# Kernel optimization log

Hardware: AMD Instinct MI355X
Metric: run time of the kernel (lower is better)

The kernel has to match this reference:

```python
import jax, jax.numpy as jnp
import numpy as np

B, S, H = 2, 2048, 1024
G, HEADS = 4, 16
HPG = HEADS // G          # heads per group = 4
HD = H // HEADS           # head_dim = 64
DG = H // G               # per-group proj dim = 256
SCALE = 1.0 / np.sqrt(HD)


def setup_inputs() -> dict:
    key = jax.random.key(0)
    ks = jax.random.split(key, 6)
    w = 0.02
    return {
        "hidden_states": jax.random.normal(ks[0], (B, S, H), dtype=jnp.float32),
        "Wq": jax.random.normal(ks[1], (G, DG, H), dtype=jnp.float32) * w,
        "bq": jnp.zeros((G, DG), dtype=jnp.float32),
        "Wk": jax.random.normal(ks[2], (G, DG, H), dtype=jnp.float32) * w,
        "bk": jnp.zeros((G, DG), dtype=jnp.float32),
        "Wv": jax.random.normal(ks[3], (G, DG, H), dtype=jnp.float32) * w,
        "bv": jnp.zeros((G, DG), dtype=jnp.float32),
        "Wo": jax.random.normal(ks[4], (H, H), dtype=jnp.float32) * w,
        "bo": jnp.zeros((H,), dtype=jnp.float32),
    }


def _proj_split(x, W, b):
    # x: [B,S,H], W: [G,DG,H], b: [G,DG] -> [B,G,HPG,S,HD]
    y = jnp.einsum("bsh,gdh->bgsd", x, W) + b[None, :, None, :]
    y = y.reshape(x.shape[0], G, x.shape[1], HPG, HD)
    return jnp.transpose(y, (0, 1, 3, 2, 4))


def reference(hidden_states, Wq, bq, Wk, bk, Wv, bv, Wo, bo):
    q = _proj_split(hidden_states, Wq, bq)  # [B,G,HPG,S,HD]
    k = _proj_split(hidden_states, Wk, bk)
    v = _proj_split(hidden_states, Wv, bv)
    scores = jnp.einsum("bghqd,bghkd->bghqk", q, k) * SCALE
    attn = jax.nn.softmax(scores.astype(jnp.float32), axis=-1).astype(v.dtype)
    ctx = jnp.einsum("bghqk,bghkd->bghqd", attn, v)  # [B,G,HPG,S,HD]
    # merge: heads ordered group-major, matching torch cat over group dim
    ctx = jnp.transpose(ctx, (0, 3, 1, 2, 4)).reshape(hidden_states.shape[0], hidden_states.shape[1], H)
    return jnp.einsum("bsh,oh->bso", ctx, Wo) + bo
```

## Files before the change

### kernel.cpp

```cpp
#include <hip/hip_runtime.h>

typedef __bf16 bf16x8 __attribute__((ext_vector_type(8)));
typedef __bf16 bf16x4 __attribute__((ext_vector_type(4)));
typedef short short4v __attribute__((ext_vector_type(4)));
typedef float f32x4 __attribute__((ext_vector_type(4)));

#define LOG2E 1.4426950408889634f

static __device__ __forceinline__ unsigned short f2bf(float f) {
  union { float f; unsigned int u; } c; c.f = f;
  return (unsigned short)((c.u + 0x7fffu + ((c.u >> 16) & 1u)) >> 16);
}

static __device__ __forceinline__ void gload16(const void* g, void* l) {
  __builtin_amdgcn_global_load_lds(
      (const __attribute__((address_space(1))) void*)g,
      (__attribute__((address_space(3))) void*)l, 16, 0, 0);
}

static __device__ __forceinline__ float exp2fast(float x) {
#if __has_builtin(__builtin_amdgcn_exp2f)
  return __builtin_amdgcn_exp2f(x);
#else
  return exp2f(x);
#endif
}

#if __has_builtin(__builtin_amdgcn_mfma_f32_16x16x16bf16_1k)
#define MFMA16_FALLBACK 0
static __device__ __forceinline__ f32x4 mfma16(bf16x4 a, bf16x4 b, f32x4 c) {
  return __builtin_amdgcn_mfma_f32_16x16x16bf16_1k(
      __builtin_bit_cast(short4v, a), __builtin_bit_cast(short4v, b), c, 0, 0, 0);
}
#else
#define MFMA16_FALLBACK 1
static __device__ __forceinline__ f32x4 mfma16(bf16x4 a, bf16x4 b, f32x4 c) {
  f32x4 d;
  asm("s_nop 1\n\tv_mfma_f32_16x16x16_bf16 %0, %1, %2, %3"
      : "=v"(d) : "v"(a), "v"(b), "v"(c));
  return d;
}
#endif

__global__ void cvt_all(const float* __restrict__ x,
                        const float* __restrict__ Wq,
                        const float* __restrict__ Wk,
                        const float* __restrict__ Wv,
                        const float* __restrict__ Wo,
                        ushort4* __restrict__ dst) {
  int i = blockIdx.x * 256 + threadIdx.x;
  const float* src;
  int off;
  if (i < 1048576) {
    src = x; off = i;
  } else {
    int t = (i - 1048576) >> 18;
    off = (i - 1048576) & 262143;
    src = (t == 0) ? Wq : (t == 1) ? Wk : (t == 2) ? Wv : Wo;
  }
  float4 f = ((const float4*)src)[off];
  ushort4 o;
  o.x = f2bf(f.x); o.y = f2bf(f.y); o.z = f2bf(f.z); o.w = f2bf(f.w);
  dst[i] = o;
}

__launch_bounds__(256, 2)
__global__ void qkv_gemm(const unsigned short* __restrict__ xb,
                         const unsigned short* __restrict__ wq,
                         const unsigned short* __restrict__ wk,
                         const unsigned short* __restrict__ wv,
                         const float* __restrict__ bq,
                         const float* __restrict__ bk,
                         const float* __restrict__ bv,
                         unsigned short* __restrict__ Qo,
                         unsigned short* __restrict__ Ko,
                         unsigned short* __restrict__ VTo) {
  __shared__ unsigned short As[128 * 64];
  __shared__ unsigned short Bs[128 * 64];
  const int s0 = blockIdx.x * 128;
  const int n0g = blockIdx.y * 128;
  const int qkv = n0g >> 10;
  const int d0 = n0g & 1023;
  const unsigned short* W = (qkv == 0) ? wq : ((qkv == 1) ? wk : wv);
  const float* bias = (qkv == 0) ? bq : ((qkv == 1) ? bk : bv);

  const unsigned short* Aptr; const unsigned short* Bptr;
  int Aoff, Boff;
  if (qkv < 2) { Aptr = W;  Aoff = d0; Bptr = xb; Boff = s0; }
  else         { Aptr = xb; Aoff = s0; Bptr = W;  Boff = d0; }

  const int tid = threadIdx.x;
  const int lane = tid & 63;
  const int wid = tid >> 6;
  const int wm = (wid >> 1) * 64;
  const int wn = (wid & 1) * 64;
  const int lm = lane & 15;
  const int quad = lane >> 4;

  f32x4 acc[4][4] = {};

  for (int kk = 0; kk < 1024; kk += 64) {
#pragma unroll
    for (int t = 0; t < 4; ++t) {
      int i = t * 256 + tid;
      int row = i >> 3, tp = i & 7;
      int seg = tp ^ (row & 7);
      gload16(Aptr + (size_t)(Aoff + row) * 1024 + kk + seg * 8,
              As + (size_t)i * 8);
      gload16(Bptr + (size_t)(Boff + row) * 1024 + kk + seg * 8,
              Bs + (size_t)i * 8);
    }
    __syncthreads();
#pragma unroll
    for (int h = 0; h < 2; ++h) {
      bf16x8 af[4], bff[4];
#pragma unroll
      for (int mt = 0; mt < 4; ++mt) {
        int r = wm + mt * 16 + lm;
        af[mt] = *(const bf16x8*)(As + r * 64 + (((h * 4 + quad) ^ (r & 7)) * 8));
      }
#pragma unroll
      for (int nt = 0; nt < 4; ++nt) {
        int r = wn + nt * 16 + lm;
        bff[nt] = *(const bf16x8*)(Bs + r * 64 + (((h * 4 + quad) ^ (r & 7)) * 8));
      }
#pragma unroll
      for (int mt = 0; mt < 4; ++mt)
#pragma unroll
        for (int nt = 0; nt < 4; ++nt)
          acc[mt][nt] = __builtin_amdgcn_mfma_f32_16x16x32_bf16(
              af[mt], bff[nt], acc[mt][nt], 0, 0, 0);
    }
    __syncthreads();
  }

  if (qkv < 2) {
    unsigned short* OUT = (qkv == 0) ? Qo : Ko;
    const float scale = (qkv == 0) ? (0.125f * LOG2E) : 1.0f;
#pragma unroll
    for (int mt = 0; mt < 4; ++mt) {
      const int d = d0 + wm + mt * 16 + quad * 4;
      const int g = d >> 8, hpg = (d >> 6) & 3, hd = d & 63;
      const float4 bb = *(const float4*)(bias + d);
#pragma unroll
      for (int nt = 0; nt < 4; ++nt) {
        const int srow = s0 + wn + nt * 16 + lm;
        const int bidx = srow >> 11, s = srow & 2047;
        const int head = (bidx * 4 + g) * 4 + hpg;
        ushort4 o;
        o.x = f2bf((acc[mt][nt][0] + bb.x) * scale);
        o.y = f2bf((acc[mt][nt][1] + bb.y) * scale);
        o.z = f2bf((acc[mt][nt][2] + bb.z) * scale);
        o.w = f2bf((acc[mt][nt][3] + bb.w) * scale);
        *(ushort4*)(OUT + (size_t)head * 131072 + (size_t)s * 64 + hd) = o;
      }
    }
  } else {
#pragma unroll
    for (int nt = 0; nt < 4; ++nt) {
      const int d = d0 + wn + nt * 16 + lm;
      const int g = d >> 8, hpg = (d >> 6) & 3, hd = d & 63;
      const float bb = bias[d];
#pragma unroll
      for (int mt = 0; mt < 4; ++mt) {
        const int sbase = s0 + wm + mt * 16 + quad * 4;
        const int bidx = sbase >> 11, s = sbase & 2047;
        const int head = (bidx * 4 + g) * 4 + hpg;
        ushort4 o;
        o.x = f2bf(acc[mt][nt][0] + bb);
        o.y = f2bf(acc[mt][nt][1] + bb);
        o.z = f2bf(acc[mt][nt][2] + bb);
        o.w = f2bf(acc[mt][nt][3] + bb);
        *(ushort4*)(VTo + (size_t)head * 131072 + (size_t)hd * 2048 + s) = o;
      }
    }
  }
}

static __device__ __forceinline__ void stage_kv(
    const unsigned short* Kh, const unsigned short* Vh, int kv0,
    unsigned short* ksl, unsigned short* vsl, int tid) {
#pragma unroll
  for (int t = 0; t < 4; ++t) {
    int i = t * 256 + tid;
    int slab = i >> 9, kv = (i >> 2) & 127, tp = i & 3;
    int tc = tp ^ ((kv >> 1) & 3);
    gload16(Kh + (size_t)(kv0 + kv) * 64 + slab * 32 + tc * 8, ksl + (size_t)i * 8);
  }
#pragma unroll
  for (int t = 0; t < 4; ++t) {
    int i = t * 256 + tid;
    int hd = i >> 4, tp = i & 15;
    int tc = tp ^ ((hd >> 1) & 7);
    gload16(Vh + (size_t)hd * 2048 + kv0 + tc * 8, vsl + (size_t)i * 8);
  }
}

__launch_bounds__(256, 2)
__global__ void attn_kernel(const unsigned short* __restrict__ Q,
                            const unsigned short* __restrict__ K,
                            const unsigned short* __restrict__ VT,
                            unsigned short* __restrict__ ctx) {
  __shared__ __align__(16) unsigned char smem[65536];

  const int head = blockIdx.y;
  const int q0 = blockIdx.x * 128;
  const int b = head >> 4;
  const int colbase = (head & 15) * 64;

  const unsigned short* Kh = K + (size_t)head * 131072;
  const unsigned short* Vh = VT + (size_t)head * 131072;

  const int tid = threadIdx.x;
  const int lane = tid & 63;
  const int w = tid >> 6;
  const int wq = w & 1;
  const int wkv = w >> 1;
  const int lm = lane & 15;
  const int quad = lane >> 4;

  bf16x8 qf[2][4];
#pragma unroll
  for (int nt = 0; nt < 4; ++nt) {
    const size_t qrow = (size_t)(q0 + wq * 64 + nt * 16 + lm);
#pragma unroll
    for (int c = 0; c < 2; ++c)
      qf[c][nt] = *(const bf16x8*)(Q + (size_t)head * 131072 + qrow * 64 +
                                   c * 32 + quad * 8);
  }

  stage_kv(Kh, Vh, 0, (unsigned short*)smem,
           (unsigned short*)(smem + 32768), tid);
  __syncthreads();

  float psum[4] = {0.f, 0.f, 0.f, 0.f};
  f32x4 oacc[4][4] = {};
  const int kchunk = (quad ^ ((lm >> 1) & 3)) * 8;

  for (int it = 0; it < 16; ++it) {
    const int buf = it & 1;
    const unsigned short* kb = (const unsigned short*)(smem + buf * 16384);
    const unsigned short* vb = (const unsigned short*)(smem + 32768 + buf * 16384);
    if (it < 15)
      stage_kv(Kh, Vh, (it + 1) * 128,
               (unsigned short*)(smem + (buf ^ 1) * 16384),
               (unsigned short*)(smem + 32768 + (buf ^ 1) * 16384), tid);

#pragma unroll
    for (int mt = 0; mt < 4; ++mt) {
      const int kvrow = wkv * 64 + mt * 16 + lm;
      f32x4 s[4] = {};
#pragma unroll
      for (int c = 0; c < 2; ++c) {
        bf16x8 kf = *(const bf16x8*)(kb + c * 4096 + kvrow * 32 + kchunk);
#pragma unroll
        for (int nt = 0; nt < 4; ++nt)
          s[nt] = __builtin_amdgcn_mfma_f32_16x16x32_bf16(kf, qf[c][nt], s[nt],
                                                          0, 0, 0);
      }
      bf16x4 pf[4];
#pragma unroll
      for (int nt = 0; nt < 4; ++nt) {
        float e0 = exp2fast(s[nt][0]), e1 = exp2fast(s[nt][1]);
        float e2 = exp2fast(s[nt][2]), e3 = exp2fast(s[nt][3]);
        psum[nt] += (e0 + e1) + (e2 + e3);
        bf16x4 t;
        t[0] = (__bf16)e0; t[1] = (__bf16)e1; t[2] = (__bf16)e2; t[3] = (__bf16)e3;
        pf[nt] = t;
      }
      const int vgran = ((wkv * 16 + mt * 4 + quad) ^ (lm & 14)) * 4;
#pragma unroll
      for (int hm = 0; hm < 4; ++hm) {
        bf16x4 vf = *(const bf16x4*)(vb + (hm * 16 + lm) * 128 + vgran);
#pragma unroll
        for (int nt = 0; nt < 4; ++nt)
          oacc[hm][nt] = mfma16(vf, pf[nt], oacc[hm][nt]);
      }
    }
    __syncthreads();
  }

#if MFMA16_FALLBACK
  asm volatile("s_nop 7\n\ts_nop 7");
#endif
#pragma unroll
  for (int nt = 0; nt < 4; ++nt) {
    psum[nt] += __shfl_xor(psum[nt], 16, 64);
    psum[nt] += __shfl_xor(psum[nt], 32, 64);
  }

  float* red = (float*)smem;
  float* psred = (float*)(smem + 34816);
  if (wkv == 1) {
#pragma unroll
    for (int nt = 0; nt < 4; ++nt) {
      const int qi = wq * 64 + nt * 16 + lm;
      if (quad == 0) psred[qi] = psum[nt];
#pragma unroll
      for (int hm = 0; hm < 4; ++hm)
        *(f32x4*)(red + qi * 68 + hm * 16 + quad * 4) = oacc[hm][nt];
    }
  }
  __syncthreads();
  if (wkv == 0) {
#pragma unroll
    for (int nt = 0; nt < 4; ++nt) {
      const int qi = wq * 64 + nt * 16 + lm;
      const float inv = 1.0f / (psum[nt] + psred[qi]);
      const size_t row = (size_t)(b * 2048 + q0 + qi);
#pragma unroll
      for (int hm = 0; hm < 4; ++hm) {
        f32x4 o = *(const f32x4*)(red + qi * 68 + hm * 16 + quad * 4);
        o += oacc[hm][nt];
        ushort4 st;
        st.x = f2bf(o[0] * inv);
        st.y = f2bf(o[1] * inv);
        st.z = f2bf(o[2] * inv);
        st.w = f2bf(o[3] * inv);
        *(ushort4*)(ctx + row * 1024 + colbase + hm * 16 + quad * 4) = st;
      }
    }
  }
}

__launch_bounds__(256, 4)
__global__ void out_gemm(const unsigned short* __restrict__ A,
                         const unsigned short* __restrict__ Wb,
                         const float* __restrict__ bo,
                         float* __restrict__ out) {
  __shared__ unsigned short As[128 * 64];
  __shared__ unsigned short Bs[64 * 64];
  const int s0 = blockIdx.x * 64;
  const int o0 = blockIdx.y * 128;

  const int tid = threadIdx.x;
  const int lane = tid & 63;
  const int wid = tid >> 6;
  const int wm = (wid >> 1) * 64;
  const int wn = (wid & 1) * 32;
  const int lm = lane & 15;
  const int quad = lane >> 4;

  f32x4 acc[4][2] = {};

  for (int kk = 0; kk < 1024; kk += 64) {
#pragma unroll
    for (int t = 0; t < 4; ++t) {
      int i = t * 256 + tid;
      int row = i >> 3, tp = i & 7;
      int seg = tp ^ (row & 7);
      gload16(Wb + (size_t)(o0 + row) * 1024 + kk + seg * 8, As + (size_t)i * 8);
    }
#pragma unroll
    for (int t = 0; t < 2; ++t) {
      int i = t * 256 + tid;
      int row = i >> 3, tp = i & 7;
      int seg = tp ^ (row & 7);
      gload16(A + (size_t)(s0 + row) * 1024 + kk + seg * 8, Bs + (size_t)i * 8);
    }
    __syncthreads();
#pragma unroll
    for (int h = 0; h < 2; ++h) {
      bf16x8 af[4], bff[2];
#pragma unroll
      for (int mt = 0; mt < 4; ++mt) {
        int r = wm + mt * 16 + lm;
        af[mt] = *(const bf16x8*)(As + r * 64 + (((h * 4 + quad) ^ (r & 7)) * 8));
      }
#pragma unroll
      for (int nt = 0; nt < 2; ++nt) {
        int r = wn + nt * 16 + lm;
        bff[nt] = *(const bf16x8*)(Bs + r * 64 + (((h * 4 + quad) ^ (r & 7)) * 8));
      }
#pragma unroll
      for (int mt = 0; mt < 4; ++mt)
#pragma unroll
        for (int nt = 0; nt < 2; ++nt)
          acc[mt][nt] = __builtin_amdgcn_mfma_f32_16x16x32_bf16(
              af[mt], bff[nt], acc[mt][nt], 0, 0, 0);
    }
    __syncthreads();
  }

#pragma unroll
  for (int mt = 0; mt < 4; ++mt) {
    const int o = o0 + wm + mt * 16 + quad * 4;
    const float4 bb = *(const float4*)(bo + o);
#pragma unroll
    for (int nt = 0; nt < 2; ++nt) {
      const int s = s0 + wn + nt * 16 + lm;
      float4 v;
      v.x = acc[mt][nt][0] + bb.x;
      v.y = acc[mt][nt][1] + bb.y;
      v.z = acc[mt][nt][2] + bb.z;
      v.w = acc[mt][nt][3] + bb.w;
      *(float4*)(out + (size_t)s * 1024 + o) = v;
    }
  }
}

extern "C" void kernel_launch(void* const* d_in, const int* in_sizes, int n_in,
                              void* d_out, int out_size, void* d_ws, size_t ws_size,
                              hipStream_t stream) {
  const float* x  = (const float*)d_in[0];
  const float* Wq = (const float*)d_in[1];
  const float* bq = (const float*)d_in[2];
  const float* Wk = (const float*)d_in[3];
  const float* bk = (const float*)d_in[4];
  const float* Wv = (const float*)d_in[5];
  const float* bv = (const float*)d_in[6];
  const float* Wo = (const float*)d_in[7];
  const float* bo = (const float*)d_in[8];
  float* out = (float*)d_out;

  char* ws = (char*)d_ws;
  unsigned short* xb  = (unsigned short*)(ws + 0);
  unsigned short* wqb = (unsigned short*)(ws + 8388608);
  unsigned short* wkb = (unsigned short*)(ws + 10485760);
  unsigned short* wvb = (unsigned short*)(ws + 12582912);
  unsigned short* wob = (unsigned short*)(ws + 14680064);
  unsigned short* Qb  = (unsigned short*)(ws + 16777216);
  unsigned short* Kb  = (unsigned short*)(ws + 25165824);
  unsigned short* VTb = (unsigned short*)(ws + 33554432);
  unsigned short* ctxb= (unsigned short*)(ws + 41943040);
  if (ws_size < 50331648) return;

  cvt_all<<<8192, 256, 0, stream>>>(x, Wq, Wk, Wv, Wo, (ushort4*)ws);
  qkv_gemm<<<dim3(32, 24), 256, 0, stream>>>(xb, wqb, wkb, wvb, bq, bk, bv,
                                             Qb, Kb, VTb);
  attn_kernel<<<dim3(16, 32), 256, 0, stream>>>(Qb, Kb, VTb, ctxb);
  out_gemm<<<dim3(64, 8), 256, 0, stream>>>(ctxb, wob, bo, out);
}
```

Measured before the change: 182.4 us.

## Fuse QKV, attention and output GEMM into one persistent kernel with grid barriers

The three compute kernels become device functions called from one persistent kernel of 512 blocks. A software grid barrier built on atomics separates the QKV projection, attention and output projection phases, with the barrier reset inside the conversion kernel. The goal is to remove launch gaps and inter-kernel drains. In exchange, the output GEMM now runs at 2 blocks per CU instead of 4, QKV tiles are imbalanced (768 tiles over 512 blocks), and the barrier relies on all 512 blocks being co-resident, or it deadlocks.

```diff
diff --git a/kernel.cpp b/kernel.cpp
--- a/kernel.cpp
+++ b/kernel.cpp
@@ -42,12 +42,36 @@
 }
 #endif
 
+static __device__ __forceinline__ void grid_barrier(unsigned* bar, unsigned nblk) {
+  __syncthreads();
+  __threadfence();
+  if (threadIdx.x == 0) {
+    unsigned gen = __hip_atomic_load(bar + 1, __ATOMIC_ACQUIRE,
+                                     __HIP_MEMORY_SCOPE_AGENT);
+    unsigned a = __hip_atomic_fetch_add(bar, 1u, __ATOMIC_ACQ_REL,
+                                        __HIP_MEMORY_SCOPE_AGENT);
+    if (a == nblk - 1u) {
+      __hip_atomic_store(bar, 0u, __ATOMIC_RELAXED, __HIP_MEMORY_SCOPE_AGENT);
+      __hip_atomic_store(bar + 1, gen + 1u, __ATOMIC_RELEASE,
+                         __HIP_MEMORY_SCOPE_AGENT);
+    } else {
+      while (__hip_atomic_load(bar + 1, __ATOMIC_ACQUIRE,
+                               __HIP_MEMORY_SCOPE_AGENT) == gen)
+        __builtin_amdgcn_s_sleep(8);
+    }
+  }
+  __threadfence();
+  __syncthreads();
+}
+
 __global__ void cvt_all(const float* __restrict__ x,
                         const float* __restrict__ Wq,
                         const float* __restrict__ Wk,
                         const float* __restrict__ Wv,
                         const float* __restrict__ Wo,
-                        ushort4* __restrict__ dst) {
+                        ushort4* __restrict__ dst,
+                        unsigned* __restrict__ bar) {
+  if (blockIdx.x == 0 && threadIdx.x < 8) bar[threadIdx.x] = 0u;
   int i = blockIdx.x * 256 + threadIdx.x;
   const float* src;
   int off;
@@ -64,21 +88,22 @@
   dst[i] = o;
 }
 
-__launch_bounds__(256, 2)
-__global__ void qkv_gemm(const unsigned short* __restrict__ xb,
-                         const unsigned short* __restrict__ wq,
-                         const unsigned short* __restrict__ wk,
-                         const unsigned short* __restrict__ wv,
-                         const float* __restrict__ bq,
-                         const float* __restrict__ bk,
-                         const float* __restrict__ bv,
-                         unsigned short* __restrict__ Qo,
-                         unsigned short* __restrict__ Ko,
-                         unsigned short* __restrict__ VTo) {
-  __shared__ unsigned short As[128 * 64];
-  __shared__ unsigned short Bs[128 * 64];
-  const int s0 = blockIdx.x * 128;
-  const int n0g = blockIdx.y * 128;
+
+static __device__ void qkv_tile(int tile, unsigned char* smem,
+                                const unsigned short* __restrict__ xb,
+                                const unsigned short* __restrict__ wq,
+                                const unsigned short* __restrict__ wk,
+                                const unsigned short* __restrict__ wv,
+                                const float* __restrict__ bq,
+                                const float* __restrict__ bk,
+                                const float* __restrict__ bv,
+                                unsigned short* __restrict__ Qo,
+                                unsigned short* __restrict__ Ko,
+                                unsigned short* __restrict__ VTo) {
+  unsigned short* As = (unsigned short*)smem;
+  unsigned short* Bs = (unsigned short*)(smem + 16384);
+  const int s0 = (tile & 31) * 128;
+  const int n0g = (tile >> 5) * 128;
   const int qkv = n0g >> 10;
   const int d0 = n0g & 1023;
   const unsigned short* W = (qkv == 0) ? wq : ((qkv == 1) ? wk : wv);
@@ -196,15 +221,13 @@
   }
 }
 
-__launch_bounds__(256, 2)
-__global__ void attn_kernel(const unsigned short* __restrict__ Q,
-                            const unsigned short* __restrict__ K,
-                            const unsigned short* __restrict__ VT,
-                            unsigned short* __restrict__ ctx) {
-  __shared__ __align__(16) unsigned char smem[65536];
-
-  const int head = blockIdx.y;
-  const int q0 = blockIdx.x * 128;
+static __device__ void attn_tile(int tile, unsigned char* smem,
+                                 const unsigned short* __restrict__ Q,
+                                 const unsigned short* __restrict__ K,
+                                 const unsigned short* __restrict__ VT,
+                                 unsigned short* __restrict__ ctx) {
+  const int head = tile >> 4;
+  const int q0 = (tile & 15) * 128;
   const int b = head >> 4;
   const int colbase = (head & 15) * 64;
 
@@ -323,15 +346,15 @@
   }
 }
 
-__launch_bounds__(256, 4)
-__global__ void out_gemm(const unsigned short* __restrict__ A,
-                         const unsigned short* __restrict__ Wb,
-                         const float* __restrict__ bo,
-                         float* __restrict__ out) {
-  __shared__ unsigned short As[128 * 64];
-  __shared__ unsigned short Bs[64 * 64];
-  const int s0 = blockIdx.x * 64;
-  const int o0 = blockIdx.y * 128;
+static __device__ void out_tile(int tile, unsigned char* smem,
+                                const unsigned short* __restrict__ A,
+                                const unsigned short* __restrict__ Wb,
+                                const float* __restrict__ bo,
+                                float* __restrict__ out) {
+  unsigned short* As = (unsigned short*)smem;
+  unsigned short* Bs = (unsigned short*)(smem + 16384);
+  const int s0 = (tile & 63) * 64;
+  const int o0 = (tile >> 6) * 128;
 
   const int tid = threadIdx.x;
   const int lane = tid & 63;
@@ -397,6 +420,36 @@
       *(float4*)(out + (size_t)s * 1024 + o) = v;
     }
   }
+}
+
+__launch_bounds__(256, 2)
+__global__ void fused_kernel(const unsigned short* __restrict__ xb,
+                             const unsigned short* __restrict__ wqb,
+                             const unsigned short* __restrict__ wkb,
+                             const unsigned short* __restrict__ wvb,
+                             const unsigned short* __restrict__ wob,
+                             const float* __restrict__ bq,
+                             const float* __restrict__ bk,
+                             const float* __restrict__ bv,
+                             const float* __restrict__ bo,
+                             unsigned short* __restrict__ Qb,
+                             unsigned short* __restrict__ Kb,
+                             unsigned short* __restrict__ VTb,
+                             unsigned short* __restrict__ ctxb,
+                             float* __restrict__ out,
+                             unsigned* __restrict__ bar) {
+  __shared__ __align__(16) unsigned char smem[65536];
+
+  for (int tile = blockIdx.x; tile < 768; tile += 512)
+    qkv_tile(tile, smem, xb, wqb, wkb, wvb, bq, bk, bv, Qb, Kb, VTb);
+
+  grid_barrier(bar, 512);
+
+  attn_tile(blockIdx.x, smem, Qb, Kb, VTb, ctxb);
+
+  grid_barrier(bar, 512);
+
+  out_tile(blockIdx.x, smem, ctxb, wob, bo, out);
 }
 
 extern "C" void kernel_launch(void* const* d_in, const int* in_sizes, int n_in,
@@ -423,11 +476,11 @@
   unsigned short* Kb  = (unsigned short*)(ws + 25165824);
   unsigned short* VTb = (unsigned short*)(ws + 33554432);
   unsigned short* ctxb= (unsigned short*)(ws + 41943040);
-  if (ws_size < 50331648) return;
-
-  cvt_all<<<8192, 256, 0, stream>>>(x, Wq, Wk, Wv, Wo, (ushort4*)ws);
-  qkv_gemm<<<dim3(32, 24), 256, 0, stream>>>(xb, wqb, wkb, wvb, bq, bk, bv,
-                                             Qb, Kb, VTb);
-  attn_kernel<<<dim3(16, 32), 256, 0, stream>>>(Qb, Kb, VTb, ctxb);
-  out_gemm<<<dim3(64, 8), 256, 0, stream>>>(ctxb, wob, bo, out);
-}
+  unsigned* bar       = (unsigned*)(ws + 50331648);
+  if (ws_size < 50331680) return;
+
+  cvt_all<<<8192, 256, 0, stream>>>(x, Wq, Wk, Wv, Wo, (ushort4*)ws, bar);
+  fused_kernel<<<512, 256, 0, stream>>>(xb, wqb, wkb, wvb, wob,
+                                        bq, bk, bv, bo,
+                                        Qb, Kb, VTb, ctxb, out, bar);
+}
```

Result: slower. 541.4 us (+196.7%).

## Double-buffer LDS tiles in QKV and output GEMMs to overlap loads

Applied to the files above, without the earlier changes.

Both GEMM kernels now keep two LDS buffers per operand. The next k-slice is issued via global_load_lds into the alternate buffer before computing on the current one, so global-to-LDS latency can hide behind MFMA work. One barrier per iteration is kept. LDS use doubles: QKV goes to 64KB and out_gemm to 48KB, and out_gemm's launch bounds drop from 4 to 3 blocks per CU. This lowers occupancy, and the waitcnt for the async loads may still serialise at the barrier.

```diff
diff --git a/kernel.cpp b/kernel.cpp
--- a/kernel.cpp
+++ b/kernel.cpp
@@ -75,8 +75,8 @@
                          unsigned short* __restrict__ Qo,
                          unsigned short* __restrict__ Ko,
                          unsigned short* __restrict__ VTo) {
-  __shared__ unsigned short As[128 * 64];
-  __shared__ unsigned short Bs[128 * 64];
+  __shared__ unsigned short As[2][8192];
+  __shared__ unsigned short Bs[2][8192];
   const int s0 = blockIdx.x * 128;
   const int n0g = blockIdx.y * 128;
   const int qkv = n0g >> 10;
@@ -99,30 +99,40 @@
 
   f32x4 acc[4][4] = {};
 
-  for (int kk = 0; kk < 1024; kk += 64) {
-#pragma unroll
-    for (int t = 0; t < 4; ++t) {
-      int i = t * 256 + tid;
-      int row = i >> 3, tp = i & 7;
-      int seg = tp ^ (row & 7);
-      gload16(Aptr + (size_t)(Aoff + row) * 1024 + kk + seg * 8,
-              As + (size_t)i * 8);
-      gload16(Bptr + (size_t)(Boff + row) * 1024 + kk + seg * 8,
-              Bs + (size_t)i * 8);
-    }
-    __syncthreads();
+#define QKV_STAGE(KK, BUF)                                                  \
+  {                                                                         \
+    _Pragma("unroll")                                                       \
+    for (int t = 0; t < 4; ++t) {                                           \
+      int i = t * 256 + tid;                                                \
+      int row = i >> 3, tp = i & 7;                                         \
+      int seg = tp ^ (row & 7);                                             \
+      gload16(Aptr + (size_t)(Aoff + row) * 1024 + (KK) + seg * 8,          \
+              &As[BUF][(size_t)i * 8]);                                     \
+      gload16(Bptr + (size_t)(Boff + row) * 1024 + (KK) + seg * 8,          \
+              &Bs[BUF][(size_t)i * 8]);                                     \
+    }                                                                       \
+  }
+
+  QKV_STAGE(0, 0);
+  __syncthreads();
+
+  for (int it = 0; it < 16; ++it) {
+    const int buf = it & 1;
+    if (it < 15) QKV_STAGE((it + 1) * 64, buf ^ 1);
 #pragma unroll
     for (int h = 0; h < 2; ++h) {
       bf16x8 af[4], bff[4];
 #pragma unroll
       for (int mt = 0; mt < 4; ++mt) {
         int r = wm + mt * 16 + lm;
-        af[mt] = *(const bf16x8*)(As + r * 64 + (((h * 4 + quad) ^ (r & 7)) * 8));
+        af[mt] = *(const bf16x8*)(&As[buf][0] + r * 64 +
+                                  (((h * 4 + quad) ^ (r & 7)) * 8));
       }
 #pragma unroll
       for (int nt = 0; nt < 4; ++nt) {
         int r = wn + nt * 16 + lm;
-        bff[nt] = *(const bf16x8*)(Bs + r * 64 + (((h * 4 + quad) ^ (r & 7)) * 8));
+        bff[nt] = *(const bf16x8*)(&Bs[buf][0] + r * 64 +
+                                   (((h * 4 + quad) ^ (r & 7)) * 8));
       }
 #pragma unroll
       for (int mt = 0; mt < 4; ++mt)
@@ -133,6 +143,7 @@
     }
     __syncthreads();
   }
+#undef QKV_STAGE
 
   if (qkv < 2) {
     unsigned short* OUT = (qkv == 0) ? Qo : Ko;
@@ -323,13 +334,13 @@
   }
 }
 
-__launch_bounds__(256, 4)
+__launch_bounds__(256, 3)
 __global__ void out_gemm(const unsigned short* __restrict__ A,
                          const unsigned short* __restrict__ Wb,
                          const float* __restrict__ bo,
                          float* __restrict__ out) {
-  __shared__ unsigned short As[128 * 64];
-  __shared__ unsigned short Bs[64 * 64];
+  __shared__ unsigned short As[2][8192];
+  __shared__ unsigned short Bs[2][4096];
   const int s0 = blockIdx.x * 64;
   const int o0 = blockIdx.y * 128;
 
@@ -343,34 +354,46 @@
 
   f32x4 acc[4][2] = {};
 
-  for (int kk = 0; kk < 1024; kk += 64) {
-#pragma unroll
-    for (int t = 0; t < 4; ++t) {
-      int i = t * 256 + tid;
-      int row = i >> 3, tp = i & 7;
-      int seg = tp ^ (row & 7);
-      gload16(Wb + (size_t)(o0 + row) * 1024 + kk + seg * 8, As + (size_t)i * 8);
-    }
-#pragma unroll
-    for (int t = 0; t < 2; ++t) {
-      int i = t * 256 + tid;
-      int row = i >> 3, tp = i & 7;
-      int seg = tp ^ (row & 7);
-      gload16(A + (size_t)(s0 + row) * 1024 + kk + seg * 8, Bs + (size_t)i * 8);
-    }
-    __syncthreads();
+#define OUT_STAGE(KK, BUF)                                                  \
+  {                                                                         \
+    _Pragma("unroll")                                                       \
+    for (int t = 0; t < 4; ++t) {                                           \
+      int i = t * 256 + tid;                                                \
+      int row = i >> 3, tp = i & 7;                                         \
+      int seg = tp ^ (row & 7);                                             \
+      gload16(Wb + (size_t)(o0 + row) * 1024 + (KK) + seg * 8,              \
+              &As[BUF][(size_t)i * 8]);                                     \
+    }                                                                       \
+    _Pragma("unroll")                                                       \
+    for (int t = 0; t < 2; ++t) {                                           \
+      int i = t * 256 + tid;                                                \
+      int row = i >> 3, tp = i & 7;                                         \
+      int seg = tp ^ (row & 7);                                             \
+      gload16(A + (size_t)(s0 + row) * 1024 + (KK) + seg * 8,               \
+              &Bs[BUF][(size_t)i * 8]);                                     \
+    }                                                                       \
+  }
+
+  OUT_STAGE(0, 0);
+  __syncthreads();
+
+  for (int it = 0; it < 16; ++it) {
+    const int buf = it & 1;
+    if (it < 15) OUT_STAGE((it + 1) * 64, buf ^ 1);
 #pragma unroll
     for (int h = 0; h < 2; ++h) {
       bf16x8 af[4], bff[2];
 #pragma unroll
       for (int mt = 0; mt < 4; ++mt) {
         int r = wm + mt * 16 + lm;
-        af[mt] = *(const bf16x8*)(As + r * 64 + (((h * 4 + quad) ^ (r & 7)) * 8));
+        af[mt] = *(const bf16x8*)(&As[buf][0] + r * 64 +
+                                  (((h * 4 + quad) ^ (r & 7)) * 8));
       }
 #pragma unroll
       for (int nt = 0; nt < 2; ++nt) {
         int r = wn + nt * 16 + lm;
-        bff[nt] = *(const bf16x8*)(Bs + r * 64 + (((h * 4 + quad) ^ (r & 7)) * 8));
+        bff[nt] = *(const bf16x8*)(&Bs[buf][0] + r * 64 +
+                                   (((h * 4 + quad) ^ (r & 7)) * 8));
       }
 #pragma unroll
       for (int mt = 0; mt < 4; ++mt)
@@ -381,6 +404,7 @@
     }
     __syncthreads();
   }
+#undef OUT_STAGE
 
 #pragma unroll
   for (int mt = 0; mt < 4; ++mt) {
```

After: 194.3 us. 6.5% more time.
